# Optimization experiments

Hardware: AMD Instinct MI355X
Metric: run time of the kernel (lower is better)

Reference implementation:

```python
import jax, jax.numpy as jnp
import numpy as np

NEG_SLOPE = 0.2  # PyG GATConv default leaky_relu slope


def gat_conv(x, src, dst, n, W, a_src, a_dst, bias, concat):
    """PyG-style GATConv (add_self_loops already applied to src/dst)."""
    H, C = a_src.shape
    h = (x @ W).reshape(n, H, C)                      # [N,H,C]
    al_src = jnp.einsum('nhc,hc->nh', h, a_src)       # [N,H]
    al_dst = jnp.einsum('nhc,hc->nh', h, a_dst)       # [N,H]
    e = jax.nn.leaky_relu(al_src[src] + al_dst[dst], NEG_SLOPE)  # [E,H]
    # segment softmax over incoming edges of each dst node
    m = jax.ops.segment_max(e, dst, num_segments=n)   # [N,H]
    ex = jnp.exp(e - m[dst])
    denom = jax.ops.segment_sum(ex, dst, num_segments=n)
    alpha = ex / denom[dst]                            # [E,H]
    out = jax.ops.segment_sum(h[src] * alpha[:, :, None], dst, num_segments=n)  # [N,H,C]
    if concat:
        out = out.reshape(n, H * C)
    else:
        out = out.mean(axis=1)
    return out + bias


def setup_inputs() -> dict:
    key = jax.random.key(0)
    ks = jax.random.split(key, 12)
    N, E = 100000, 1600000
    IN, HID, OUT, H = 128, 16, 32, 4
    x = jax.random.normal(ks[0], (N, IN), dtype=jnp.float32)
    edge_index = jax.random.randint(ks[1], (2, E), 0, N, dtype=jnp.int64)
    s = 0.1
    W1 = jax.random.normal(ks[2], (IN, H * HID), dtype=jnp.float32) * s
    a_src1 = jax.random.normal(ks[3], (H, HID), dtype=jnp.float32) * s
    a_dst1 = jax.random.normal(ks[4], (H, HID), dtype=jnp.float32) * s
    b1 = jnp.zeros((H * HID,), dtype=jnp.float32)
    W2 = jax.random.normal(ks[5], (H * HID, H * OUT), dtype=jnp.float32) * s
    a_src2 = jax.random.normal(ks[6], (H, OUT), dtype=jnp.float32) * s
    a_dst2 = jax.random.normal(ks[7], (H, OUT), dtype=jnp.float32) * s
    b2 = jnp.zeros((OUT,), dtype=jnp.float32)
    return {"x": x, "edge_index": edge_index,
            "W1": W1, "a_src1": a_src1, "a_dst1": a_dst1, "b1": b1,
            "W2": W2, "a_src2": a_src2, "a_dst2": a_dst2, "b2": b2}


def reference(x, edge_index, W1, a_src1, a_dst1, b1, W2, a_src2, a_dst2, b2):
    n = x.shape[0]
    loop = jnp.arange(n, dtype=edge_index.dtype)
    src = jnp.concatenate([edge_index[0], loop])
    dst = jnp.concatenate([edge_index[1], loop])
    # dropout is identity at inference
    h = gat_conv(x, src, dst, n, W1, a_src1, a_dst1, b1, concat=True)
    h = gat_conv(h, src, dst, n, W2, a_src2, a_dst2, b2, concat=False)
    h = jax.nn.elu(h)
    return jax.nn.log_softmax(h, axis=1)
```

## Files before the change

kernel.cpp:

```cpp
#include <hip/hip_runtime.h>
#include <hip/hip_fp16.h>
#include <cstdint>
#include <cstddef>

#define NEG 0.2f
#define TILE 4096
#define WEXP(e) __expf((e) > 0.f ? (e) : NEG * (e))

typedef int i4v __attribute__((ext_vector_type(4)));

__device__ __forceinline__ i4v ld_i4(const int* p) {
    i4v r;
    __builtin_memcpy(&r, p, 16);
    return r;
}
__device__ __forceinline__ __half2 bch(unsigned v) { __half2 r; *(unsigned*)&r = v; return r; }
__device__ __forceinline__ __half2 bchi(int v) { __half2 r; *(int*)&r = v; return r; }


__global__ __launch_bounds__(256) void bhist_k(const int* __restrict__ ei, int* __restrict__ bc, int E, int nbk) {
    __shared__ int sb[256];
    int t = threadIdx.x;
    sb[t] = 0;
    __syncthreads();
    int stride = gridDim.x * 256;
    for (int i = blockIdx.x * 256 + t; i < E; i += stride) {
        int d = __builtin_nontemporal_load(ei + E + i);
        atomicAdd(&sb[d >> 9], 1);
    }
    __syncthreads();
    if (t < nbk && sb[t] > 0) atomicAdd(&bc[t], sb[t]);
}


__global__ __launch_bounds__(256) void bscan_k(const int* __restrict__ bc, int* __restrict__ bb,
                                               int* __restrict__ curA, int nbk) {
    __shared__ int sm[256];
    int t = threadIdx.x;
    int v = (t < nbk) ? bc[t] : 0;
    sm[t] = v; __syncthreads();
    for (int off = 1; off < 256; off <<= 1) {
        int u = (t >= off) ? sm[t - off] : 0;
        __syncthreads();
        sm[t] += u;
        __syncthreads();
    }
    if (t < nbk) {
        int ex = sm[t] - v;
        bb[t] = ex;
        curA[t] = ex;
        if (t == nbk - 1) bb[nbk] = sm[t];
    }
}


__global__ __launch_bounds__(256) void partA_k(const int* __restrict__ ei, int* __restrict__ curA,
                                               uint2* __restrict__ pairs, int E, int nbk) {
    __shared__ int scnt[256];
    __shared__ int sc[256];
    __shared__ int sbase[256];
    __shared__ int gbase[256];
    __shared__ int cur2[256];
    __shared__ int ssrc[TILE];
    __shared__ int sdst[TILE];
    int t = threadIdx.x;
    int ntiles = (E + TILE - 1) / TILE;
    for (int tile = blockIdx.x; tile < ntiles; tile += gridDim.x) {
        int base = tile * TILE;
        int cntE = min(TILE, E - base);
        scnt[t] = 0;
        __syncthreads();
        int mys[16], myd[16];
        #pragma unroll
        for (int j = 0; j < 16; j++) {
            int i = base + t + 256 * j;
            int s = 0, d = -1;
            if (i < E) {
                s = __builtin_nontemporal_load(ei + i);
                d = __builtin_nontemporal_load(ei + E + i);
            }
            mys[j] = s; myd[j] = d;
            if (d >= 0) atomicAdd(&scnt[d >> 9], 1);
        }
        __syncthreads();
        sc[t] = scnt[t];
        __syncthreads();
        for (int off = 1; off < 256; off <<= 1) {
            int u = (t >= off) ? sc[t - off] : 0;
            __syncthreads();
            sc[t] += u;
            __syncthreads();
        }
        int myb = sc[t] - scnt[t];
        sbase[t] = myb;
        cur2[t] = myb;
        if (t < nbk && scnt[t] > 0) gbase[t] = atomicAdd(&curA[t], scnt[t]);
        __syncthreads();
        #pragma unroll
        for (int j = 0; j < 16; j++) {
            int d = myd[j];
            if (d >= 0) {
                int b = d >> 9;
                int pos = atomicAdd(&cur2[b], 1);
                ssrc[pos] = mys[j];
                sdst[pos] = d;
            }
        }
        __syncthreads();
        for (int i = t; i < cntE; i += 256) {
            int d = sdst[i];
            int b = d >> 9;
            int addr = gbase[b] + (i - sbase[b]);
            pairs[addr] = make_uint2((unsigned)ssrc[i], (unsigned)d);
        }
        __syncthreads();
    }
}


__global__ __launch_bounds__(256) void partB2_k(const uint2* __restrict__ pin, const int* __restrict__ bb,
                                                int* __restrict__ rp, int* __restrict__ cnt,
                                                int* __restrict__ srcout, int N) {
    __shared__ int cur[512];
    __shared__ int sc[512];
    int b = blockIdx.x, t = threadIdx.x;
    int d0 = b << 9;
    cur[t] = 0; cur[t + 256] = 0;
    __syncthreads();
    int ebase = bb[b], eend = bb[b + 1];
    for (int j = ebase + t; j < eend; j += 256) {
        int d = (int)pin[j].y;
        atomicAdd(&cur[d - d0], 1);
    }
    __syncthreads();
    sc[t] = cur[t]; sc[t + 256] = cur[t + 256];
    __syncthreads();
    for (int off = 1; off <= 256; off <<= 1) {
        int a0 = (t >= off) ? sc[t - off] : 0;
        int a1 = sc[t + 256 - off];
        __syncthreads();
        sc[t] += a0; sc[t + 256] += a1;
        __syncthreads();
    }
    int base0 = ebase + sc[t] - cur[t];
    int base1 = ebase + sc[t + 256] - cur[t + 256];
    if (d0 + t < N)       { rp[d0 + t] = base0;       cnt[d0 + t] = cur[t]; }
    if (d0 + t + 256 < N) { rp[d0 + t + 256] = base1; cnt[d0 + t + 256] = cur[t + 256]; }
    cur[t] = base0; cur[t + 256] = base1;
    __syncthreads();
    for (int j = ebase + t; j < eend; j += 256) {
        uint2 p = pin[j];
        int d = (int)p.y;
        int pos = atomicAdd(&cur[d - d0], 1);
        srcout[pos] = (int)p.x;
    }
}


__global__ __launch_bounds__(256) void gemm1_k(const float* __restrict__ x, const float* __restrict__ W,
                                               const float* __restrict__ a_src, const float* __restrict__ a_dst,
                                               __half* __restrict__ h, float* __restrict__ alsrc,
                                               float* __restrict__ aldst, int N) {
    __shared__ float Bs[128 * 64];
    __shared__ float xs[64][68];
    int t = threadIdx.x;
    for (int i = t; i < 128 * 64 / 4; i += 256)
        ((float4*)Bs)[i] = ((const float4*)W)[i];
    int ct = t & 15, rt = t >> 4;
    int head = ct >> 2, cq = ct & 3;
    float asv[4], adv[4];
    #pragma unroll
    for (int j = 0; j < 4; j++) {
        asv[j] = a_src[head * 16 + 4 * cq + j];
        adv[j] = a_dst[head * 16 + 4 * cq + j];
    }
    int ntiles = (N + 63) >> 6;
    for (int tile = blockIdx.x; tile < ntiles; tile += gridDim.x) {
        int r0 = tile << 6;
        float acc[4][4];
        #pragma unroll
        for (int i = 0; i < 4; i++)
            #pragma unroll
            for (int j = 0; j < 4; j++) acc[i][j] = 0.f;
        for (int kc = 0; kc < 128; kc += 64) {
            __syncthreads();
            int srow = t >> 4, sf4 = t & 15;
            #pragma unroll
            for (int p = 0; p < 4; p++) {
                int r = r0 + srow + 16 * p;
                float4 v = make_float4(0.f, 0.f, 0.f, 0.f);
                if (r < N) v = *(const float4*)(x + (size_t)r * 128 + kc + 4 * sf4);
                *(float4*)&xs[srow + 16 * p][4 * sf4] = v;
            }
            __syncthreads();
            #pragma unroll 4
            for (int k = 0; k < 64; k++) {
                float4 bv = *(float4*)&Bs[(kc + k) * 64 + 4 * ct];
                #pragma unroll
                for (int i = 0; i < 4; i++) {
                    float xv = xs[4 * rt + i][k];
                    acc[i][0] = fmaf(xv, bv.x, acc[i][0]);
                    acc[i][1] = fmaf(xv, bv.y, acc[i][1]);
                    acc[i][2] = fmaf(xv, bv.z, acc[i][2]);
                    acc[i][3] = fmaf(xv, bv.w, acc[i][3]);
                }
            }
        }
        #pragma unroll
        for (int i = 0; i < 4; i++) {
            int r = r0 + 4 * rt + i;
            float ps = 0.f, pd = 0.f;
            #pragma unroll
            for (int j = 0; j < 4; j++) {
                ps = fmaf(acc[i][j], asv[j], ps);
                pd = fmaf(acc[i][j], adv[j], pd);
            }
            ps += __shfl_xor(ps, 1); ps += __shfl_xor(ps, 2);
            pd += __shfl_xor(pd, 1); pd += __shfl_xor(pd, 2);
            if (r < N) {
                __half2 h0 = __floats2half2_rn(acc[i][0], acc[i][1]);
                __half2 h1 = __floats2half2_rn(acc[i][2], acc[i][3]);
                *(__half2*)(h + (size_t)r * 64 + 4 * ct) = h0;
                *(__half2*)(h + (size_t)r * 64 + 4 * ct + 2) = h1;
                if (cq == 0) { alsrc[r * 4 + head] = ps; aldst[r * 4 + head] = pd; }
            }
        }
    }
}


__global__ __launch_bounds__(256) void prew_k(const float* __restrict__ W2, const float* __restrict__ as2,
                                              const float* __restrict__ ad2, float* __restrict__ was,
                                              float* __restrict__ wad) {
    int t = threadIdx.x;
    int k = t >> 2, hh = t & 3;
    const float* wrow = W2 + k * 128 + hh * 32;
    const float* av = as2 + hh * 32;
    const float* dv = ad2 + hh * 32;
    float s = 0.f, ds = 0.f;
    #pragma unroll 8
    for (int c = 0; c < 32; c++) {
        float w = wrow[c];
        s = fmaf(w, av[c], s);
        ds = fmaf(w, dv[c], ds);
    }
    was[t] = s;
    wad[t] = ds;
}


__global__ __launch_bounds__(256) void node1_k(const __half* __restrict__ h, const int* __restrict__ srccol,
                                               const float* __restrict__ alsrc, const float* __restrict__ aldst,
                                               const int* __restrict__ rp, const int* __restrict__ cnt,
                                               const float* __restrict__ bias,
                                               const float* __restrict__ was, const float* __restrict__ wad,
                                               __half* __restrict__ out,
                                               float* __restrict__ alsrc2, float* __restrict__ aldst2, int N) {
    int t = threadIdx.x;
    int d = (blockIdx.x * 256 + t) >> 4;
    if (d >= N) return;
    int c = t & 15;
    int eh = c >> 2, hh = c & 3;
    int mh = c >> 2;
    const uint2* hb = (const uint2*)h;
    float myad = aldst[d * 4 + hh];
    float selfw = WEXP(alsrc[d * 4 + hh] + myad);
    __half2 sh2 = __float2half2_rn(selfw);
    int si = *(int*)&sh2;
    float mden = (eh == 0) ? selfw : 0.f;
    uint2 u = hb[((size_t)d << 4) + c];
    __half2 smy = bchi(__shfl(si, mh, 16));
    __half2 acc0 = __hmul2(smy, bch(u.x));
    __half2 acc1 = __hmul2(smy, bch(u.y));
    int start = rp[d], deg = cnt[d];
    int nq = deg >> 2;
    int i = 0;
    #define N1_PROC(G0, G1, G2, G3, AW) { \
        float w_ = WEXP((AW) + myad); \
        mden += w_; \
        __half2 wh_ = __float2half2_rn(w_); \
        int wi_ = *(int*)&wh_; \
        __half2 q0_ = bchi(__shfl(wi_, 0 + mh, 16)); \
        __half2 q1_ = bchi(__shfl(wi_, 4 + mh, 16)); \
        __half2 q2_ = bchi(__shfl(wi_, 8 + mh, 16)); \
        __half2 q3_ = bchi(__shfl(wi_, 12 + mh, 16)); \
        acc0 = __hfma2(q0_, bch(G0.x), acc0); acc1 = __hfma2(q0_, bch(G0.y), acc1); \
        acc0 = __hfma2(q1_, bch(G1.x), acc0); acc1 = __hfma2(q1_, bch(G1.y), acc1); \
        acc0 = __hfma2(q2_, bch(G2.x), acc0); acc1 = __hfma2(q2_, bch(G2.y), acc1); \
        acc0 = __hfma2(q3_, bch(G3.x), acc0); acc1 = __hfma2(q3_, bch(G3.y), acc1); }
    if (nq > 0) {
        i4v sv = ld_i4(srccol + start);
        uint2 g0 = hb[((size_t)(unsigned)sv.x << 4) + c];
        uint2 g1 = hb[((size_t)(unsigned)sv.y << 4) + c];
        uint2 g2 = hb[((size_t)(unsigned)sv.z << 4) + c];
        uint2 g3 = hb[((size_t)(unsigned)sv.w << 4) + c];
        int my = (eh == 0) ? sv.x : (eh == 1) ? sv.y : (eh == 2) ? sv.z : sv.w;
        float aw = alsrc[(size_t)my * 4 + hh];
        i4v nv = (nq > 1) ? ld_i4(srccol + start + 4) : sv;
        for (int q = 1; q < nq; q++) {
            uint2 n0 = hb[((size_t)(unsigned)nv.x << 4) + c];
            uint2 n1 = hb[((size_t)(unsigned)nv.y << 4) + c];
            uint2 n2 = hb[((size_t)(unsigned)nv.z << 4) + c];
            uint2 n3 = hb[((size_t)(unsigned)nv.w << 4) + c];
            int nmy = (eh == 0) ? nv.x : (eh == 1) ? nv.y : (eh == 2) ? nv.z : nv.w;
            float naw = alsrc[(size_t)nmy * 4 + hh];
            i4v nv2 = (q + 1 < nq) ? ld_i4(srccol + start + 4 * (q + 1)) : nv;
            N1_PROC(g0, g1, g2, g3, aw)
            g0 = n0; g1 = n1; g2 = n2; g3 = n3; aw = naw; nv = nv2;
        }
        N1_PROC(g0, g1, g2, g3, aw)
        i = nq << 2;
    }
    for (; i < deg; i++) {
        int s = srccol[start + i];
        uint2 us = hb[((size_t)(unsigned)s << 4) + c];
        float w = WEXP(alsrc[(size_t)s * 4 + hh] + myad);
        mden += (eh == 0) ? w : 0.f;
        __half2 wh = __float2half2_rn(w);
        int wi = *(int*)&wh;
        __half2 qq = bchi(__shfl(wi, mh, 16));
        acc0 = __hfma2(qq, bch(us.x), acc0);
        acc1 = __hfma2(qq, bch(us.y), acc1);
    }
    mden += __shfl_xor(mden, 4, 16);
    mden += __shfl_xor(mden, 8, 16);
    float den = __shfl(mden, mh, 16);
    float inv = 1.f / den;
    float2 f0 = __half22float2(acc0), f1 = __half22float2(acc1);
    float4 b = *(const float4*)(bias + 4 * c);
    float v0 = f0.x * inv + b.x, v1 = f0.y * inv + b.y;
    float v2 = f1.x * inv + b.z, v3 = f1.y * inv + b.w;
    __half2 o0 = __floats2half2_rn(v0, v1);
    __half2 o1 = __floats2half2_rn(v2, v3);
    uint2 o; o.x = *(unsigned*)&o0; o.y = *(unsigned*)&o1;
    *(uint2*)(out + (size_t)d * 64 + 4 * c) = o;
    const float4* was4 = (const float4*)was;
    const float4* wad4 = (const float4*)wad;
    float4 wa0 = was4[4 * c + 0], wa1 = was4[4 * c + 1], wa2 = was4[4 * c + 2], wa3 = was4[4 * c + 3];
    float4 wd0 = wad4[4 * c + 0], wd1 = wad4[4 * c + 1], wd2 = wad4[4 * c + 2], wd3 = wad4[4 * c + 3];
    float4 ps, pd;
    ps.x = fmaf(v0, wa0.x, fmaf(v1, wa1.x, fmaf(v2, wa2.x, v3 * wa3.x)));
    ps.y = fmaf(v0, wa0.y, fmaf(v1, wa1.y, fmaf(v2, wa2.y, v3 * wa3.y)));
    ps.z = fmaf(v0, wa0.z, fmaf(v1, wa1.z, fmaf(v2, wa2.z, v3 * wa3.z)));
    ps.w = fmaf(v0, wa0.w, fmaf(v1, wa1.w, fmaf(v2, wa2.w, v3 * wa3.w)));
    pd.x = fmaf(v0, wd0.x, fmaf(v1, wd1.x, fmaf(v2, wd2.x, v3 * wd3.x)));
    pd.y = fmaf(v0, wd0.y, fmaf(v1, wd1.y, fmaf(v2, wd2.y, v3 * wd3.y)));
    pd.z = fmaf(v0, wd0.z, fmaf(v1, wd1.z, fmaf(v2, wd2.z, v3 * wd3.z)));
    pd.w = fmaf(v0, wd0.w, fmaf(v1, wd1.w, fmaf(v2, wd2.w, v3 * wd3.w)));
    #pragma unroll
    for (int off = 1; off <= 8; off <<= 1) {
        ps.x += __shfl_xor(ps.x, off); ps.y += __shfl_xor(ps.y, off);
        ps.z += __shfl_xor(ps.z, off); ps.w += __shfl_xor(ps.w, off);
        pd.x += __shfl_xor(pd.x, off); pd.y += __shfl_xor(pd.y, off);
        pd.z += __shfl_xor(pd.z, off); pd.w += __shfl_xor(pd.w, off);
    }
    if (c == 0) {
        *(float4*)(alsrc2 + (size_t)d * 4) = ps;
        *(float4*)(aldst2 + (size_t)d * 4) = pd;
    }
}


#define EDGE_SH(J, U) { \
    __half2 l_ = bch(U.x), h_ = bch(U.y); \
    __half2 qa = bchi(__shfl(wi, 4 * J + 0, 16)); \
    __half2 qb = bchi(__shfl(wi, 4 * J + 1, 16)); \
    __half2 qc = bchi(__shfl(wi, 4 * J + 2, 16)); \
    __half2 qd = bchi(__shfl(wi, 4 * J + 3, 16)); \
    aA0 = __hfma2(qa, l_, aA0); aA1 = __hfma2(qa, h_, aA1); \
    aB0 = __hfma2(qb, l_, aB0); aB1 = __hfma2(qb, h_, aB1); \
    aC0 = __hfma2(qc, l_, aC0); aC1 = __hfma2(qc, h_, aC1); \
    aD0 = __hfma2(qd, l_, aD0); aD1 = __hfma2(qd, h_, aD1); }

__global__ __launch_bounds__(256) void node2_k(const __half* __restrict__ h1o, const int* __restrict__ srccol,
                                               const float* __restrict__ alsrc, const float* __restrict__ aldst,
                                               const int* __restrict__ rp, const int* __restrict__ cnt,
                                               __half* __restrict__ y, int N) {
    int t = threadIdx.x;
    int d = (blockIdx.x * 256 + t) >> 4;
    if (d >= N) return;
    int c = t & 15;
    int eh = c >> 2;
    int hh = c & 3;
    const uint2* hb = (const uint2*)h1o;
    float myad = aldst[d * 4 + hh];
    float selfw = WEXP(alsrc[d * 4 + hh] + myad);
    __half2 selfh = __float2half2_rn(selfw);
    int selfi = *(int*)&selfh;
    float mden = (eh == 0) ? selfw : 0.f;
    uint2 u = hb[((size_t)d << 4) + c];
    __half2 lo = bch(u.x), hi = bch(u.y);
    __half2 sA = bchi(__shfl(selfi, 0, 16));
    __half2 sB = bchi(__shfl(selfi, 1, 16));
    __half2 sC = bchi(__shfl(selfi, 2, 16));
    __half2 sD = bchi(__shfl(selfi, 3, 16));
    __half2 aA0 = __hmul2(sA, lo), aA1 = __hmul2(sA, hi);
    __half2 aB0 = __hmul2(sB, lo), aB1 = __hmul2(sB, hi);
    __half2 aC0 = __hmul2(sC, lo), aC1 = __hmul2(sC, hi);
    __half2 aD0 = __hmul2(sD, lo), aD1 = __hmul2(sD, hi);
    int start = rp[d], deg = cnt[d];
    int nq = deg >> 2;
    int i = 0;
    #define N2_PROC(G0, G1, G2, G3, AW) { \
        float w_ = WEXP((AW) + myad); \
        mden += w_; \
        __half2 wh_ = __float2half2_rn(w_); \
        int wi = *(int*)&wh_; \
        EDGE_SH(0, G0) EDGE_SH(1, G1) EDGE_SH(2, G2) EDGE_SH(3, G3) }
    if (nq > 0) {
        i4v sv = ld_i4(srccol + start);
        uint2 g0 = hb[((size_t)(unsigned)sv.x << 4) + c];
        uint2 g1 = hb[((size_t)(unsigned)sv.y << 4) + c];
        uint2 g2 = hb[((size_t)(unsigned)sv.z << 4) + c];
        uint2 g3 = hb[((size_t)(unsigned)sv.w << 4) + c];
        int my = (eh == 0) ? sv.x : (eh == 1) ? sv.y : (eh == 2) ? sv.z : sv.w;
        float aw = alsrc[(size_t)my * 4 + hh];
        i4v nv = (nq > 1) ? ld_i4(srccol + start + 4) : sv;
        for (int q = 1; q < nq; q++) {
            uint2 n0 = hb[((size_t)(unsigned)nv.x << 4) + c];
            uint2 n1 = hb[((size_t)(unsigned)nv.y << 4) + c];
            uint2 n2 = hb[((size_t)(unsigned)nv.z << 4) + c];
            uint2 n3 = hb[((size_t)(unsigned)nv.w << 4) + c];
            int nmy = (eh == 0) ? nv.x : (eh == 1) ? nv.y : (eh == 2) ? nv.z : nv.w;
            float naw = alsrc[(size_t)nmy * 4 + hh];
            i4v nv2 = (q + 1 < nq) ? ld_i4(srccol + start + 4 * (q + 1)) : nv;
            N2_PROC(g0, g1, g2, g3, aw)
            g0 = n0; g1 = n1; g2 = n2; g3 = n3; aw = naw; nv = nv2;
        }
        N2_PROC(g0, g1, g2, g3, aw)
        i = nq << 2;
    }
    for (; i < deg; i++) {
        int s = srccol[start + i];
        uint2 us = hb[((size_t)(unsigned)s << 4) + c];
        float w = WEXP(alsrc[(size_t)s * 4 + hh] + myad);
        mden += (eh == 0) ? w : 0.f;
        __half2 wh = __float2half2_rn(w);
        int wi = *(int*)&wh;
        EDGE_SH(0, us)
    }
    mden += __shfl_xor(mden, 4, 16);
    mden += __shfl_xor(mden, 8, 16);
    float dnA = __shfl(mden, 0, 16);
    float dnB = __shfl(mden, 1, 16);
    float dnC = __shfl(mden, 2, 16);
    float dnD = __shfl(mden, 3, 16);
    __half2 jA = __float2half2_rn(0.25f / dnA), jB = __float2half2_rn(0.25f / dnB);
    __half2 jC = __float2half2_rn(0.25f / dnC), jD = __float2half2_rn(0.25f / dnD);
    uint2 oA, oB, oC, oD;
    ((__half2*)&oA)[0] = __hmul2(jA, aA0); ((__half2*)&oA)[1] = __hmul2(jA, aA1);
    ((__half2*)&oB)[0] = __hmul2(jB, aB0); ((__half2*)&oB)[1] = __hmul2(jB, aB1);
    ((__half2*)&oC)[0] = __hmul2(jC, aC0); ((__half2*)&oC)[1] = __hmul2(jC, aC1);
    ((__half2*)&oD)[0] = __hmul2(jD, aD0); ((__half2*)&oD)[1] = __hmul2(jD, aD1);
    __half* yp = y + (size_t)d * 256 + 4u * (unsigned)c;
    *(uint2*)(yp)       = oA;
    *(uint2*)(yp + 64)  = oB;
    *(uint2*)(yp + 128) = oC;
    *(uint2*)(yp + 192) = oD;
}


__global__ __launch_bounds__(256) void gemm3_k(const __half* __restrict__ y, const float* __restrict__ W2,
                                               const float* __restrict__ bias, float* __restrict__ out, int N) {
    __shared__ unsigned wk[128 * 32];
    __shared__ unsigned ys[32 * 130];
    int t = threadIdx.x;
    for (int i = t; i < 4096; i += 256) {
        int k2 = i >> 5, col = i & 31;
        int hh = k2 >> 5, kk = (2 * k2) & 63;
        float f0 = W2[kk * 128 + hh * 32 + col];
        float f1 = W2[(kk + 1) * 128 + hh * 32 + col];
        __half2 hv = __floats2half2_rn(f0, f1);
        wk[i] = *(unsigned*)&hv;
    }
    int ct = t & 7, rt = t >> 3;
    float4 b4 = *(const float4*)(bias + 4 * ct);
    int r0 = blockIdx.x << 5;
    for (int i = t; i < 32 * 64; i += 256) {
        int row = i >> 6, k4 = i & 63;
        uint2 v = make_uint2(0u, 0u);
        int r = r0 + row;
        if (r < N) v = *(const uint2*)(y + (size_t)r * 256 + 4 * k4);
        *(uint2*)&ys[row * 130 + 2 * k4] = v;
    }
    __syncthreads();
    float acc[4] = {0.f, 0.f, 0.f, 0.f};
    const unsigned* yr = ys + rt * 130;
    const unsigned* wp = wk + 4 * ct;
    for (int kc = 0; kc < 128; kc += 16) {
        __half2 h0 = __float2half2_rn(0.f), h1 = h0, h2 = h0, h3 = h0;
        #pragma unroll
        for (int j = 0; j < 16; j++) {
            int k2 = kc + j;
            __half2 x2 = bch(yr[k2]);
            uint2 w01 = *(const uint2*)&wp[k2 * 32];
            uint2 w23 = *(const uint2*)&wp[k2 * 32 + 2];
            h0 = __hfma2(x2, bch(w01.x), h0);
            h1 = __hfma2(x2, bch(w01.y), h1);
            h2 = __hfma2(x2, bch(w23.x), h2);
            h3 = __hfma2(x2, bch(w23.y), h3);
        }
        float2 q0 = __half22float2(h0), q1 = __half22float2(h1);
        float2 q2 = __half22float2(h2), q3 = __half22float2(h3);
        acc[0] += q0.x + q0.y;
        acc[1] += q1.x + q1.y;
        acc[2] += q2.x + q2.y;
        acc[3] += q3.x + q3.y;
    }
    int row = r0 + rt;
    float ev0 = acc[0] + b4.x;
    float ev1 = acc[1] + b4.y;
    float ev2 = acc[2] + b4.z;
    float ev3 = acc[3] + b4.w;
    ev0 = ev0 > 0.f ? ev0 : __expf(ev0) - 1.f;
    ev1 = ev1 > 0.f ? ev1 : __expf(ev1) - 1.f;
    ev2 = ev2 > 0.f ? ev2 : __expf(ev2) - 1.f;
    ev3 = ev3 > 0.f ? ev3 : __expf(ev3) - 1.f;
    float mx = fmaxf(fmaxf(ev0, ev1), fmaxf(ev2, ev3));
    #pragma unroll
    for (int off = 1; off <= 4; off <<= 1) mx = fmaxf(mx, __shfl_xor(mx, off));
    float sm = __expf(ev0 - mx) + __expf(ev1 - mx) + __expf(ev2 - mx) + __expf(ev3 - mx);
    #pragma unroll
    for (int off = 1; off <= 4; off <<= 1) sm += __shfl_xor(sm, off);
    float ls = mx + __logf(sm);
    if (row < N) {
        float4 o;
        o.x = ev0 - ls; o.y = ev1 - ls; o.z = ev2 - ls; o.w = ev3 - ls;
        *(float4*)(out + (size_t)row * 32 + 4 * ct) = o;
    }
}


extern "C" void kernel_launch(void* const* d_in, const int* in_sizes, int n_in,
                              void* d_out, int out_size, void* d_ws, size_t ws_size,
                              hipStream_t stream) {
    const float* x   = (const float*)d_in[0];
    const int*   ei  = (const int*)d_in[1];
    const float* W1  = (const float*)d_in[2];
    const float* as1 = (const float*)d_in[3];
    const float* ad1 = (const float*)d_in[4];
    const float* b1  = (const float*)d_in[5];
    const float* W2  = (const float*)d_in[6];
    const float* as2 = (const float*)d_in[7];
    const float* ad2 = (const float*)d_in[8];
    const float* b2  = (const float*)d_in[9];
    float* out = (float*)d_out;
    int N = in_sizes[0] / 128;
    int E = in_sizes[1] / 2;

    char* base = (char*)d_ws;
    size_t off = 0;
    auto alloc = [&](size_t bytes) -> char* {
        char* p = base + off;
        off = (off + bytes + 255) & ~(size_t)255;
        return p;
    };
    __half* y     = (__half*)alloc((size_t)N * 256 * 2);
    __half* h1h   = (__half*)y;
    uint2*  pairs = (uint2*)((char*)y + (size_t)N * 64 * 2);
    __half* h1o   = (__half*)alloc((size_t)N * 64 * 2);
    float* alsrc1 = (float*)alloc((size_t)N * 4 * 4);
    float* aldst1 = (float*)alloc((size_t)N * 4 * 4);
    float* alsrc2 = (float*)alloc((size_t)N * 4 * 4);
    float* aldst2 = (float*)alloc((size_t)N * 4 * 4);
    float* was    = (float*)alloc(256 * 4);
    float* wad    = (float*)alloc(256 * 4);
    int* cnt  = (int*)alloc((size_t)N * 4);
    int* rp   = (int*)alloc((size_t)N * 4);
    int* curA = (int*)alloc(256 * 4);
    int* bc   = (int*)alloc(256 * 4);
    int* bb   = (int*)alloc(260 * 4);
    int* srccol = (int*)alloc((size_t)E * 4);

    int nbk = (N + 511) >> 9;
    int ntilesA = (E + TILE - 1) / TILE;
    int nt1 = (N + 63) >> 6;
    int nt3 = (N + 31) >> 5;

    prew_k<<<1, 256, 0, stream>>>(W2, as2, ad2, was, wad);
    hipMemsetAsync(bc, 0, 256 * 4, stream);
    bhist_k<<<512, 256, 0, stream>>>(ei, bc, E, nbk);
    bscan_k<<<1, 256, 0, stream>>>(bc, bb, curA, nbk);
    partA_k<<<ntilesA, 256, 0, stream>>>(ei, curA, pairs, E, nbk);
    partB2_k<<<nbk, 256, 0, stream>>>(pairs, bb, rp, cnt, srccol, N);

    gemm1_k<<<(nt1 + 1) / 2, 256, 0, stream>>>(x, W1, as1, ad1, h1h, alsrc1, aldst1, N);
    node1_k<<<(N + 15) / 16, 256, 0, stream>>>(h1h, srccol, alsrc1, aldst1, rp, cnt, b1,
                                               was, wad, h1o, alsrc2, aldst2, N);
    node2_k<<<(N + 15) / 16, 256, 0, stream>>>(h1o, srccol, alsrc2, aldst2, rp, cnt, y, N);
    gemm3_k<<<nt3, 256, 0, stream>>>(y, W2, b2, out, N);
}
```

Before: 333.1 us.

## Fuse layer-2 projection and log-softmax into node2, transpose gemm1 x tile

The final GEMM with W2, bias, ELU and log-softmax move into the node2 aggregation kernel, using a half-precision W2 layout prepacked by prew_k and staged in shared memory. This removes the N×256 half intermediate y, its global write and reread, and the gemm3 launch. gemm1 now stores the x tile transposed with a swizzle so each k step reads one float4 instead of four scalar loads. The trade-off is heavier per-thread work in node2: 32 half2 accumulators, 16-lane shuffle reductions, and a 17 KB shared table loaded by every block, which may cut occupancy. A redundant read of rp is also added in partB2.

```diff
diff --git a/kernel.cpp b/kernel.cpp
--- a/kernel.cpp
+++ b/kernel.cpp
@@ -151,7 +151,8 @@
     for (int j = ebase + t; j < eend; j += 256) {
         uint2 p = pin[j];
         int d = (int)p.y;
-        int pos = atomicAdd(&cur[d - d0], 1);
+        int pos = rp[d] + 0;
+        pos = atomicAdd(&cur[d - d0], 1);
         srcout[pos] = (int)p.x;
     }
 }
@@ -162,7 +163,7 @@
                                                __half* __restrict__ h, float* __restrict__ alsrc,
                                                float* __restrict__ aldst, int N) {
     __shared__ float Bs[128 * 64];
-    __shared__ float xs[64][68];
+    __shared__ float xt[64 * 68];
     int t = threadIdx.x;
     for (int i = t; i < 128 * 64 / 4; i += 256)
         ((float4*)Bs)[i] = ((const float4*)W)[i];
@@ -190,20 +191,34 @@
                 int r = r0 + srow + 16 * p;
                 float4 v = make_float4(0.f, 0.f, 0.f, 0.f);
                 if (r < N) v = *(const float4*)(x + (size_t)r * 128 + kc + 4 * sf4);
-                *(float4*)&xs[srow + 16 * p][4 * sf4] = v;
+                int rr = srow + 16 * p, k0 = 4 * sf4;
+                int colb = 4 * (((rr >> 2) + sf4) & 15) + (rr & 3);
+                xt[(k0 + 0) * 68 + colb] = v.x;
+                xt[(k0 + 1) * 68 + colb] = v.y;
+                xt[(k0 + 2) * 68 + colb] = v.z;
+                xt[(k0 + 3) * 68 + colb] = v.w;
             }
             __syncthreads();
             #pragma unroll 4
             for (int k = 0; k < 64; k++) {
                 float4 bv = *(float4*)&Bs[(kc + k) * 64 + 4 * ct];
-                #pragma unroll
-                for (int i = 0; i < 4; i++) {
-                    float xv = xs[4 * rt + i][k];
-                    acc[i][0] = fmaf(xv, bv.x, acc[i][0]);
-                    acc[i][1] = fmaf(xv, bv.y, acc[i][1]);
-                    acc[i][2] = fmaf(xv, bv.z, acc[i][2]);
-                    acc[i][3] = fmaf(xv, bv.w, acc[i][3]);
-                }
+                float4 xv = *(float4*)&xt[k * 68 + 4 * ((rt + (k >> 2)) & 15)];
+                acc[0][0] = fmaf(xv.x, bv.x, acc[0][0]);
+                acc[0][1] = fmaf(xv.x, bv.y, acc[0][1]);
+                acc[0][2] = fmaf(xv.x, bv.z, acc[0][2]);
+                acc[0][3] = fmaf(xv.x, bv.w, acc[0][3]);
+                acc[1][0] = fmaf(xv.y, bv.x, acc[1][0]);
+                acc[1][1] = fmaf(xv.y, bv.y, acc[1][1]);
+                acc[1][2] = fmaf(xv.y, bv.z, acc[1][2]);
+                acc[1][3] = fmaf(xv.y, bv.w, acc[1][3]);
+                acc[2][0] = fmaf(xv.z, bv.x, acc[2][0]);
+                acc[2][1] = fmaf(xv.z, bv.y, acc[2][1]);
+                acc[2][2] = fmaf(xv.z, bv.z, acc[2][2]);
+                acc[2][3] = fmaf(xv.z, bv.w, acc[2][3]);
+                acc[3][0] = fmaf(xv.w, bv.x, acc[3][0]);
+                acc[3][1] = fmaf(xv.w, bv.y, acc[3][1]);
+                acc[3][2] = fmaf(xv.w, bv.z, acc[3][2]);
+                acc[3][3] = fmaf(xv.w, bv.w, acc[3][3]);
             }
         }
         #pragma unroll
@@ -231,7 +246,7 @@
 
 __global__ __launch_bounds__(256) void prew_k(const float* __restrict__ W2, const float* __restrict__ as2,
                                               const float* __restrict__ ad2, float* __restrict__ was,
-                                              float* __restrict__ wad) {
+                                              float* __restrict__ wad, unsigned* __restrict__ wkh) {
     int t = threadIdx.x;
     int k = t >> 2, hh = t & 3;
     const float* wrow = W2 + k * 128 + hh * 32;
@@ -246,6 +261,18 @@
     }
     was[t] = s;
     wad[t] = ds;
+    #pragma unroll
+    for (int j = 0; j < 16; j++) {
+        int e = t * 16 + j;
+        int r = e >> 6, cc = e & 63;
+        int col = cc >> 1, par = cc & 1;
+        int p = 2 * r + par;
+        int h = p >> 5, kk = (2 * p) & 63;
+        float f0 = W2[kk * 128 + h * 32 + col];
+        float f1 = W2[(kk + 1) * 128 + h * 32 + col];
+        __half2 hv = __floats2half2_rn(f0, f1);
+        wkh[e] = *(unsigned*)&hv;
+    }
 }
 
 
@@ -375,8 +402,16 @@
 __global__ __launch_bounds__(256) void node2_k(const __half* __restrict__ h1o, const int* __restrict__ srccol,
                                                const float* __restrict__ alsrc, const float* __restrict__ aldst,
                                                const int* __restrict__ rp, const int* __restrict__ cnt,
-                                               __half* __restrict__ y, int N) {
+                                               const unsigned* __restrict__ wkh, const float* __restrict__ b2,
+                                               float* __restrict__ out, int N) {
+    __shared__ unsigned wkl[64 * 68];
     int t = threadIdx.x;
+    #pragma unroll
+    for (int j = 0; j < 16; j++) {
+        int g = t * 16 + j;
+        wkl[(g >> 6) * 68 + (g & 63)] = wkh[g];
+    }
+    __syncthreads();
     int d = (blockIdx.x * 256 + t) >> 4;
     if (d >= N) return;
     int c = t & 15;
@@ -447,86 +482,62 @@
     float dnD = __shfl(mden, 3, 16);
     __half2 jA = __float2half2_rn(0.25f / dnA), jB = __float2half2_rn(0.25f / dnB);
     __half2 jC = __float2half2_rn(0.25f / dnC), jD = __float2half2_rn(0.25f / dnD);
-    uint2 oA, oB, oC, oD;
-    ((__half2*)&oA)[0] = __hmul2(jA, aA0); ((__half2*)&oA)[1] = __hmul2(jA, aA1);
-    ((__half2*)&oB)[0] = __hmul2(jB, aB0); ((__half2*)&oB)[1] = __hmul2(jB, aB1);
-    ((__half2*)&oC)[0] = __hmul2(jC, aC0); ((__half2*)&oC)[1] = __hmul2(jC, aC1);
-    ((__half2*)&oD)[0] = __hmul2(jD, aD0); ((__half2*)&oD)[1] = __hmul2(jD, aD1);
-    __half* yp = y + (size_t)d * 256 + 4u * (unsigned)c;
-    *(uint2*)(yp)       = oA;
-    *(uint2*)(yp + 64)  = oB;
-    *(uint2*)(yp + 128) = oC;
-    *(uint2*)(yp + 192) = oD;
-}
-
-
-__global__ __launch_bounds__(256) void gemm3_k(const __half* __restrict__ y, const float* __restrict__ W2,
-                                               const float* __restrict__ bias, float* __restrict__ out, int N) {
-    __shared__ unsigned wk[128 * 32];
-    __shared__ unsigned ys[32 * 130];
-    int t = threadIdx.x;
-    for (int i = t; i < 4096; i += 256) {
-        int k2 = i >> 5, col = i & 31;
-        int hh = k2 >> 5, kk = (2 * k2) & 63;
-        float f0 = W2[kk * 128 + hh * 32 + col];
-        float f1 = W2[(kk + 1) * 128 + hh * 32 + col];
-        __half2 hv = __floats2half2_rn(f0, f1);
-        wk[i] = *(unsigned*)&hv;
-    }
-    int ct = t & 7, rt = t >> 3;
-    float4 b4 = *(const float4*)(bias + 4 * ct);
-    int r0 = blockIdx.x << 5;
-    for (int i = t; i < 32 * 64; i += 256) {
-        int row = i >> 6, k4 = i & 63;
-        uint2 v = make_uint2(0u, 0u);
-        int r = r0 + row;
-        if (r < N) v = *(const uint2*)(y + (size_t)r * 256 + 4 * k4);
-        *(uint2*)&ys[row * 130 + 2 * k4] = v;
-    }
-    __syncthreads();
-    float acc[4] = {0.f, 0.f, 0.f, 0.f};
-    const unsigned* yr = ys + rt * 130;
-    const unsigned* wp = wk + 4 * ct;
-    for (int kc = 0; kc < 128; kc += 16) {
-        __half2 h0 = __float2half2_rn(0.f), h1 = h0, h2 = h0, h3 = h0;
+    __half2 y00 = __hmul2(jA, aA0), y01 = __hmul2(jA, aA1);
+    __half2 y10 = __hmul2(jB, aB0), y11 = __hmul2(jB, aB1);
+    __half2 y20 = __hmul2(jC, aC0), y21 = __hmul2(jC, aC1);
+    __half2 y30 = __hmul2(jD, aD0), y31 = __hmul2(jD, aD1);
+    __half2 acc[32];
+    __half2 hz = __float2half2_rn(0.f);
+    #pragma unroll
+    for (int j = 0; j < 32; j++) acc[j] = hz;
+    #define EPI_H(H, P0, P1) { \
+        const unsigned* wr = wkl + (16 * H + c) * 68; \
+        _Pragma("unroll") \
+        for (int i2 = 0; i2 < 16; i2++) { \
+            uint4 w = *(const uint4*)&wr[4 * i2]; \
+            acc[2 * i2]     = __hfma2(P0, bch(w.x), acc[2 * i2]); \
+            acc[2 * i2]     = __hfma2(P1, bch(w.y), acc[2 * i2]); \
+            acc[2 * i2 + 1] = __hfma2(P0, bch(w.z), acc[2 * i2 + 1]); \
+            acc[2 * i2 + 1] = __hfma2(P1, bch(w.w), acc[2 * i2 + 1]); \
+        } }
+    EPI_H(0, y00, y01)
+    EPI_H(1, y10, y11)
+    EPI_H(2, y20, y21)
+    EPI_H(3, y30, y31)
+    float o[32];
+    #pragma unroll
+    for (int j = 0; j < 32; j++) {
+        float2 f = __half22float2(acc[j]);
+        o[j] = f.x + f.y;
+    }
+    #pragma unroll
+    for (int off = 1; off <= 8; off <<= 1) {
         #pragma unroll
-        for (int j = 0; j < 16; j++) {
-            int k2 = kc + j;
-            __half2 x2 = bch(yr[k2]);
-            uint2 w01 = *(const uint2*)&wp[k2 * 32];
-            uint2 w23 = *(const uint2*)&wp[k2 * 32 + 2];
-            h0 = __hfma2(x2, bch(w01.x), h0);
-            h1 = __hfma2(x2, bch(w01.y), h1);
-            h2 = __hfma2(x2, bch(w23.x), h2);
-            h3 = __hfma2(x2, bch(w23.y), h3);
-        }
-        float2 q0 = __half22float2(h0), q1 = __half22float2(h1);
-        float2 q2 = __half22float2(h2), q3 = __half22float2(h3);
-        acc[0] += q0.x + q0.y;
-        acc[1] += q1.x + q1.y;
-        acc[2] += q2.x + q2.y;
-        acc[3] += q3.x + q3.y;
-    }
-    int row = r0 + rt;
-    float ev0 = acc[0] + b4.x;
-    float ev1 = acc[1] + b4.y;
-    float ev2 = acc[2] + b4.z;
-    float ev3 = acc[3] + b4.w;
-    ev0 = ev0 > 0.f ? ev0 : __expf(ev0) - 1.f;
-    ev1 = ev1 > 0.f ? ev1 : __expf(ev1) - 1.f;
-    ev2 = ev2 > 0.f ? ev2 : __expf(ev2) - 1.f;
-    ev3 = ev3 > 0.f ? ev3 : __expf(ev3) - 1.f;
-    float mx = fmaxf(fmaxf(ev0, ev1), fmaxf(ev2, ev3));
-    #pragma unroll
-    for (int off = 1; off <= 4; off <<= 1) mx = fmaxf(mx, __shfl_xor(mx, off));
-    float sm = __expf(ev0 - mx) + __expf(ev1 - mx) + __expf(ev2 - mx) + __expf(ev3 - mx);
-    #pragma unroll
-    for (int off = 1; off <= 4; off <<= 1) sm += __shfl_xor(sm, off);
+        for (int j = 0; j < 32; j++) o[j] += __shfl_xor(o[j], off, 16);
+    }
+    #pragma unroll
+    for (int j = 0; j < 32; j++) {
+        float e = o[j] + b2[j];
+        o[j] = e > 0.f ? e : __expf(e) - 1.f;
+    }
+    float mx = o[0];
+    #pragma unroll
+    for (int j = 1; j < 32; j++) mx = fmaxf(mx, o[j]);
+    float sm = 0.f;
+    #pragma unroll
+    for (int j = 0; j < 32; j++) sm += __expf(o[j] - mx);
     float ls = mx + __logf(sm);
-    if (row < N) {
-        float4 o;
-        o.x = ev0 - ls; o.y = ev1 - ls; o.z = ev2 - ls; o.w = ev3 - ls;
-        *(float4*)(out + (size_t)row * 32 + 4 * ct) = o;
+    float* op = out + (size_t)d * 32;
+    #pragma unroll
+    for (int g = 0; g < 8; g++) {
+        if (c == g) {
+            float4 v;
+            v.x = o[4 * g + 0] - ls;
+            v.y = o[4 * g + 1] - ls;
+            v.z = o[4 * g + 2] - ls;
+            v.w = o[4 * g + 3] - ls;
+            *(float4*)(op + 4 * g) = v;
+        }
     }
 }
 
@@ -555,16 +566,16 @@
         off = (off + bytes + 255) & ~(size_t)255;
         return p;
     };
-    __half* y     = (__half*)alloc((size_t)N * 256 * 2);
-    __half* h1h   = (__half*)y;
-    uint2*  pairs = (uint2*)((char*)y + (size_t)N * 64 * 2);
+    __half* h1h   = (__half*)alloc((size_t)N * 64 * 2);
     __half* h1o   = (__half*)alloc((size_t)N * 64 * 2);
+    uint2*  pairs = (uint2*)alloc((size_t)E * 8);
     float* alsrc1 = (float*)alloc((size_t)N * 4 * 4);
     float* aldst1 = (float*)alloc((size_t)N * 4 * 4);
     float* alsrc2 = (float*)alloc((size_t)N * 4 * 4);
     float* aldst2 = (float*)alloc((size_t)N * 4 * 4);
     float* was    = (float*)alloc(256 * 4);
     float* wad    = (float*)alloc(256 * 4);
+    unsigned* wkh = (unsigned*)alloc(4096 * 4);
     int* cnt  = (int*)alloc((size_t)N * 4);
     int* rp   = (int*)alloc((size_t)N * 4);
     int* curA = (int*)alloc(256 * 4);
@@ -575,9 +586,8 @@
     int nbk = (N + 511) >> 9;
     int ntilesA = (E + TILE - 1) / TILE;
     int nt1 = (N + 63) >> 6;
-    int nt3 = (N + 31) >> 5;
-
-    prew_k<<<1, 256, 0, stream>>>(W2, as2, ad2, was, wad);
+
+    prew_k<<<1, 256, 0, stream>>>(W2, as2, ad2, was, wad, wkh);
     hipMemsetAsync(bc, 0, 256 * 4, stream);
     bhist_k<<<512, 256, 0, stream>>>(ei, bc, E, nbk);
     bscan_k<<<1, 256, 0, stream>>>(bc, bb, curA, nbk);
@@ -587,6 +597,6 @@
     gemm1_k<<<(nt1 + 1) / 2, 256, 0, stream>>>(x, W1, as1, ad1, h1h, alsrc1, aldst1, N);
     node1_k<<<(N + 15) / 16, 256, 0, stream>>>(h1h, srccol, alsrc1, aldst1, rp, cnt, b1,
                                                was, wad, h1o, alsrc2, aldst2, N);
-    node2_k<<<(N + 15) / 16, 256, 0, stream>>>(h1o, srccol, alsrc2, aldst2, rp, cnt, y, N);
-    gemm3_k<<<nt3, 256, 0, stream>>>(y, W2, b2, out, N);
-}
+    node2_k<<<(N + 15) / 16, 256, 0, stream>>>(h1o, srccol, alsrc2, aldst2, rp, cnt,
+                                               wkh, b2, out, N);
+}
```

After: 331.2 us. About the same (-0.6%).
